# Performance work log

Measured on AMD Instinct MI355X. Metric: run time of the kernel, lower is better.

## Reference

```python
import jax, jax.numpy as jnp
import numpy as np

HIDDEN = 256
MAX_LENGTH = 256
NUM_LAYERS = 4
VOCAB = 50257


def setup_inputs() -> dict:
    key = jax.random.key(0)
    ks = jax.random.split(key, 16)
    s = 0.05
    return {
        "token": jax.random.randint(ks[0], (1,), 0, VOCAB, dtype=jnp.int64 if jax.config.jax_enable_x64 else jnp.int32),
        "hidden": jax.random.normal(ks[1], (NUM_LAYERS, 1, HIDDEN), dtype=jnp.float32),
        "encoder_outputs": jax.random.normal(ks[2], (MAX_LENGTH, HIDDEN), dtype=jnp.float32),
        "emb": jax.random.normal(ks[3], (VOCAB, HIDDEN), dtype=jnp.float32) * s,
        "attn_w": jax.random.normal(ks[4], (MAX_LENGTH, 2 * HIDDEN), dtype=jnp.float32) * s,
        "attn_b": jax.random.normal(ks[5], (MAX_LENGTH,), dtype=jnp.float32) * s,
        "comb_w": jax.random.normal(ks[6], (HIDDEN, 2 * HIDDEN), dtype=jnp.float32) * s,
        "comb_b": jax.random.normal(ks[7], (HIDDEN,), dtype=jnp.float32) * s,
        "gru_wih": jax.random.normal(ks[8], (NUM_LAYERS, 3 * HIDDEN, HIDDEN), dtype=jnp.float32) * s,
        "gru_whh": jax.random.normal(ks[9], (NUM_LAYERS, 3 * HIDDEN, HIDDEN), dtype=jnp.float32) * s,
        "gru_bih": jax.random.normal(ks[10], (NUM_LAYERS, 3 * HIDDEN), dtype=jnp.float32) * s,
        "gru_bhh": jax.random.normal(ks[11], (NUM_LAYERS, 3 * HIDDEN), dtype=jnp.float32) * s,
        "out_w": jax.random.normal(ks[12], (VOCAB, HIDDEN), dtype=jnp.float32) * s,
        "out_b": jax.random.normal(ks[13], (VOCAB,), dtype=jnp.float32) * s,
    }


def _gru_cell(x, h, wih, whh, bih, bhh):
    # PyTorch GRU cell: gates ordered [r, z, n]
    gi = x @ wih.T + bih  # [1, 3H]
    gh = h @ whh.T + bhh  # [1, 3H]
    i_r, i_z, i_n = jnp.split(gi, 3, axis=1)
    h_r, h_z, h_n = jnp.split(gh, 3, axis=1)
    r = jax.nn.sigmoid(i_r + h_r)
    z = jax.nn.sigmoid(i_z + h_z)
    n = jnp.tanh(i_n + r * h_n)
    return (1.0 - z) * n + z * h


def reference(token, hidden, encoder_outputs, emb, attn_w, attn_b, comb_w, comb_b,
              gru_wih, gru_whh, gru_bih, gru_bhh, out_w, out_b):
    # embedding lookup (dropout is identity in eval)  -> [1, H]
    embedded = emb[token]
    # Bahdanau-style attention weights over MAX_LENGTH positions
    attn_in = jnp.concatenate([embedded, hidden[0]], axis=1)  # [1, 2H]
    attn_weights = jax.nn.softmax(attn_in @ attn_w.T + attn_b, axis=1)  # [1, L]
    attn_applied = attn_weights @ encoder_outputs  # [1, H]
    comb_in = jnp.concatenate([embedded, attn_applied], axis=1)  # [1, 2H]
    x = jax.nn.relu(comb_in @ comb_w.T + comb_b)  # [1, H]
    # 4-layer GRU, single timestep
    new_h = []
    for l in range(NUM_LAYERS):
        h_l = _gru_cell(x, hidden[l], gru_wih[l], gru_whh[l], gru_bih[l], gru_bhh[l])
        new_h.append(h_l)
        x = h_l
    hidden_new = jnp.stack(new_h, axis=0)  # [4, 1, H]
    logp = jax.nn.log_softmax(x @ out_w.T + out_b, axis=1)  # [1, V]
    return (logp, hidden_new, attn_weights)
```

## Files before the change

kernel.cpp:

```cpp
#include <hip/hip_runtime.h>
#include <hip/hip_bf16.h>

#define H 256
#define L2H 512
#define NLAYERS 4
#define VOCAB 50257

#define OUT_LOGP 0
#define OUT_HID  50257
#define OUT_ATTN 51281

#define WS_SCORE 0
#define WS_BARS  256
#define WS_APP   512
#define WS_XA    768
#define WS_XB    1024
#define WS_PM    768
#define WS_PS    1024
#define WS_X4    1280
#define WS_GO    2048
#define WS_FLAG  2304

#define PH_SCORE 0
#define PH_APP   1
#define PH_X0    2
#define PH_LOG   7

#define NCHAIN 64
#define NBLK   256

typedef unsigned short u16;
typedef unsigned long long u64;

__device__ __forceinline__ float bf2f(u16 u) {
    return __uint_as_float(((unsigned int)u) << 16);
}

__device__ __forceinline__ u16 f2bf(float f) {
    unsigned int x = __float_as_uint(f);
    unsigned int r = x + 0x7fff + ((x >> 16) & 1);
    return (u16)(r >> 16);
}

template<bool BF16>
__device__ __forceinline__ float ld1(const void* p, size_t i) {
    if (BF16) return bf2f(((const u16*)p)[i]);
    else      return ((const float*)p)[i];
}

template<bool BF16>
__device__ __forceinline__ float4 ld4(const void* p, size_t i) {
    if (BF16) {
        ushort4 w = *(const ushort4*)((const u16*)p + i);
        return make_float4(bf2f(w.x), bf2f(w.y), bf2f(w.z), bf2f(w.w));
    } else {
        return *(const float4*)((const float*)p + i);
    }
}

template<bool BF16>
__device__ __forceinline__ void ld8(const void* p, size_t i, float* f) {
    if (BF16) {
        uint4 u = *(const uint4*)((const u16*)p + i);
        f[0] = bf2f(u.x & 0xffff); f[1] = bf2f(u.x >> 16);
        f[2] = bf2f(u.y & 0xffff); f[3] = bf2f(u.y >> 16);
        f[4] = bf2f(u.z & 0xffff); f[5] = bf2f(u.z >> 16);
        f[6] = bf2f(u.w & 0xffff); f[7] = bf2f(u.w >> 16);
    } else {
        const float4* q = (const float4*)((const float*)p + i);
        float4 a = q[0], b = q[1];
        f[0] = a.x; f[1] = a.y; f[2] = a.z; f[3] = a.w;
        f[4] = b.x; f[5] = b.y; f[6] = b.z; f[7] = b.w;
    }
}

template<bool BF16>
__device__ __forceinline__ void st(void* p, size_t i, float v) {
    if (BF16) ((u16*)p)[i] = f2bf(v);
    else      ((float*)p)[i] = v;
}

__device__ __forceinline__ float ldc(const float* p) {
    return __hip_atomic_load(const_cast<float*>(p), __ATOMIC_RELAXED, __HIP_MEMORY_SCOPE_AGENT);
}
__device__ __forceinline__ void stc(float* p, float v) {
    __hip_atomic_store(p, v, __ATOMIC_RELAXED, __HIP_MEMORY_SCOPE_AGENT);
}
__device__ __forceinline__ u64 ldcu(const u64* p) {
    return __hip_atomic_load(const_cast<u64*>(p), __ATOMIC_RELAXED, __HIP_MEMORY_SCOPE_AGENT);
}
__device__ __forceinline__ void stcu(u64* p, u64 v) {
    __hip_atomic_store(p, v, __ATOMIC_RELAXED, __HIP_MEMORY_SCOPE_AGENT);
}

__device__ __forceinline__ void stage256(float* sh, const float* src, int tid) {
    if (tid < 128) {
        u64 u = ldcu((const u64*)src + tid);
        sh[2 * tid]     = __uint_as_float((unsigned)(u & 0xffffffffull));
        sh[2 * tid + 1] = __uint_as_float((unsigned)(u >> 32));
    }
    __syncthreads();
}

__device__ __forceinline__ void arrive_ph(unsigned* bars, int bx, int ph) {
    __syncthreads();
    if (threadIdx.x == 0)
        __hip_atomic_fetch_add(&bars[(bx & 15) * 16 + ph], 1u,
                               __ATOMIC_RELAXED, __HIP_MEMORY_SCOPE_AGENT);
}
template<int SLP>
__device__ __forceinline__ void wait_ph(unsigned* bars, int ph, unsigned exp) {
    if (threadIdx.x < 16) {
        while (__hip_atomic_load(&bars[threadIdx.x * 16 + ph],
                                 __ATOMIC_RELAXED, __HIP_MEMORY_SCOPE_AGENT) < exp)
            __builtin_amdgcn_s_sleep(SLP);
    }
    __syncthreads();
}

template<int SLP>
__device__ __forceinline__ u64 poll_go(const u64* p, unsigned need) {
    u64 u = ldcu(p);
    while ((unsigned)(u & 0xffffffffull) < need) {
        __builtin_amdgcn_s_sleep(SLP);
        u = ldcu(p);
    }
    return u;
}

__device__ __forceinline__ float dot8_u4bf(uint4 u, const float* xf) {
    return bf2f(u.x & 0xffff)*xf[0] + bf2f(u.x >> 16)*xf[1]
         + bf2f(u.y & 0xffff)*xf[2] + bf2f(u.y >> 16)*xf[3]
         + bf2f(u.z & 0xffff)*xf[4] + bf2f(u.z >> 16)*xf[5]
         + bf2f(u.w & 0xffff)*xf[6] + bf2f(u.w >> 16)*xf[7];
}

__global__ __launch_bounds__(256) void k_init(const void* emb, float* ws) {
    int tid = threadIdx.x;
    __hip_atomic_store((unsigned*)(ws + WS_BARS) + tid, 0u, __ATOMIC_RELAXED, __HIP_MEMORY_SCOPE_AGENT);
    __hip_atomic_store((unsigned*)(ws + WS_GO) + tid, 0u, __ATOMIC_RELAXED, __HIP_MEMORY_SCOPE_AGENT);
    __hip_atomic_store((unsigned*)(ws + WS_APP) + tid, 0u, __ATOMIC_RELAXED, __HIP_MEMORY_SCOPE_AGENT);
    if (tid < 64) {
        float b = fabsf(bf2f(((const u16*)emb)[tid]));
        #pragma unroll
        for (int off = 32; off; off >>= 1) b = fmaxf(b, __shfl_xor(b, off));
        if (tid == 0) ws[WS_FLAG] = (b < 1.0f) ? 1.0f : 0.0f;
    }
}

template<bool BF16>
__device__ __forceinline__ void logits_stream(
    const void* __restrict__ out_w, const void* __restrict__ out_b,
    const float* xf, int grp, int l32, float* vs, float& m, float& s)
{
    #pragma unroll
    for (int it = 0; it < 3; ++it) {
        const int rb = it * 16384 + grp;
        float wf[8][8], bb[8];
        #pragma unroll
        for (int k = 0; k < 8; ++k) {
            ld8<BF16>(out_w, (size_t)(rb + (k << 11)) * H + l32 * 8, wf[k]);
            bb[k] = ld1<BF16>(out_b, rb + (k << 11));
        }
        #pragma unroll
        for (int k = 0; k < 8; ++k) {
            float v = wf[k][0]*xf[0] + wf[k][1]*xf[1] + wf[k][2]*xf[2] + wf[k][3]*xf[3]
                    + wf[k][4]*xf[4] + wf[k][5]*xf[5] + wf[k][6]*xf[6] + wf[k][7]*xf[7];
            #pragma unroll
            for (int off = 16; off; off >>= 1) v += __shfl_xor(v, off);
            v += bb[k];
            vs[it * 8 + k] = v;
            float mn = fmaxf(m, v);
            s = s * __expf(m - mn) + __expf(v - mn);
            m = mn;
        }
    }
    vs[24] = 0.f;
    if (grp < VOCAB - 49152) {
        int r = 49152 + grp;
        float wf[8]; ld8<BF16>(out_w, (size_t)r * H + l32 * 8, wf);
        float v = wf[0]*xf[0] + wf[1]*xf[1] + wf[2]*xf[2] + wf[3]*xf[3]
                + wf[4]*xf[4] + wf[5]*xf[5] + wf[6]*xf[6] + wf[7]*xf[7];
        #pragma unroll
        for (int off = 16; off; off >>= 1) v += __shfl_xor(v, off);
        v += ld1<BF16>(out_b, r);
        vs[24] = v;
        float mn = fmaxf(m, v);
        s = s * __expf(m - mn) + __expf(v - mn);
        m = mn;
    }
}

template<bool BF16>
__device__ __forceinline__ void pipeline(
    const int* __restrict__ tok, const void* __restrict__ emb,
    const void* __restrict__ hidden,
    const void* __restrict__ attn_w, const void* __restrict__ attn_b,
    const void* __restrict__ enc,
    const void* __restrict__ comb_w, const void* __restrict__ comb_b,
    const void* __restrict__ gwih, const void* __restrict__ gwhh,
    const void* __restrict__ gbih, const void* __restrict__ gbhh,
    const void* __restrict__ out_w, const void* __restrict__ out_b,
    float* __restrict__ ws, void* __restrict__ out)
{
    unsigned* bars = (unsigned*)(ws + WS_BARS);
    const int tid  = threadIdx.x;
    const int lane = tid & 63;
    const int wid  = tid >> 6;
    const int bx   = blockIdx.x;
    const size_t es = BF16 ? 2 : 4;

    const int grp = (bx << 3) | (tid >> 5);
    const int l32 = tid & 31;

    __shared__ float lds[256];
    __shared__ float xsh[256];
    __shared__ float wsm[256];
    __shared__ float cshare;

    float vs[25];
    float m = -1e30f, s = 0.f;

    if (bx < NCHAIN) {
        const int wv = (bx << 2) | wid;
        const int j8 = lane * 8;
        const int tk = tok[0];

        {
            float wf[8]; ld8<BF16>(attn_w, (size_t)wv * L2H + j8, wf);
            float xin[8];
            if (lane < 32) ld8<BF16>(emb, (size_t)tk * H + j8, xin);
            else           ld8<BF16>(hidden, (size_t)(j8 - H), xin);
            float v = 0.f;
            #pragma unroll
            for (int q = 0; q < 8; ++q) v += xin[q] * wf[q];
            #pragma unroll
            for (int off = 32; off; off >>= 1) v += __shfl_xor(v, off);
            if (lane == 0) stc(ws + WS_SCORE + wv, v + ld1<BF16>(attn_b, wv));
        }
        arrive_ph(bars, bx, PH_SCORE);

        if (bx < 16) {
            const int l0 = bx * 16;
            float ev[16];
            #pragma unroll
            for (int k = 0; k < 16; ++k)
                ev[k] = ld1<BF16>(enc, (size_t)(l0 + k) * H + tid);
            wait_ph<1>(bars, PH_SCORE, 4);
            stage256(lds, ws + WS_SCORE, tid);
            float sc = lds[tid];
            __syncthreads();
            for (int off = 128; off; off >>= 1) {
                if (tid < off) lds[tid] = fmaxf(lds[tid], lds[tid + off]);
                __syncthreads();
            }
            float M = lds[0]; __syncthreads();
            float e = __expf(sc - M);
            lds[tid] = e; __syncthreads();
            for (int off = 128; off; off >>= 1) {
                if (tid < off) lds[tid] += lds[tid + off];
                __syncthreads();
            }
            float w = e / lds[0];
            wsm[tid] = w; __syncthreads();
            if (bx == 0) st<BF16>(out, OUT_ATTN + tid, w);
            float acc = 0.f;
            #pragma unroll
            for (int k = 0; k < 16; ++k) acc += wsm[l0 + k] * ev[k];
            atomicAdd(&ws[WS_APP + tid], acc);
            arrive_ph(bars, bx, PH_APP);
        }

        {
            float wf[8]; ld8<BF16>(comb_w, (size_t)wv * L2H + j8, wf);
            float xin[8];
            if (lane < 32) ld8<BF16>(emb, (size_t)tk * H + j8, xin);
            wait_ph<1>(bars, PH_APP, 1);
            stage256(xsh, ws + WS_APP, tid);
            if (lane >= 32) {
                #pragma unroll
                for (int q = 0; q < 8; ++q) xin[q] = xsh[j8 - H + q];
            }
            float v = 0.f;
            #pragma unroll
            for (int q = 0; q < 8; ++q) v += xin[q] * wf[q];
            #pragma unroll
            for (int off = 32; off; off >>= 1) v += __shfl_xor(v, off);
            if (lane == 0) stc(ws + WS_XA + wv, fmaxf(v + ld1<BF16>(comb_b, wv), 0.f));
        }
        arrive_ph(bars, bx, PH_X0);

        const int e4 = lane * 4;
        #pragma unroll 1
        for (int l = 0; l < NLAYERS; ++l) {
            const float* xin_p = ws + ((l & 1) ? WS_XB : WS_XA);
            float*       xout  = ws + ((l & 1) ? WS_XA : WS_XB);
            const char* wih = (const char*)gwih + (size_t)l * 3 * H * H * es;
            const char* whh = (const char*)gwhh + (size_t)l * 3 * H * H * es;
            const char* bih = (const char*)gbih + (size_t)l * 3 * H * es;
            const char* bhh = (const char*)gbhh + (size_t)l * 3 * H * es;
            const char* hprev = (const char*)hidden + (size_t)l * H * es;
            char*       hout  = (char*)out + (size_t)(OUT_HID + l * H) * es;
            const int i = wv;

            float4 hv  = ld4<BF16>(hprev, e4);
            float4 wri = ld4<BF16>(wih, (size_t)(i        ) * H + e4);
            float4 wzi = ld4<BF16>(wih, (size_t)(H + i    ) * H + e4);
            float4 wni = ld4<BF16>(wih, (size_t)(2 * H + i) * H + e4);
            float4 wrh = ld4<BF16>(whh, (size_t)(i        ) * H + e4);
            float4 wzh = ld4<BF16>(whh, (size_t)(H + i    ) * H + e4);
            float4 wnh = ld4<BF16>(whh, (size_t)(2 * H + i) * H + e4);

            wait_ph<1>(bars, PH_X0 + l, 4);
            stage256(xsh, xin_p, tid);

            float4 xv;
            xv.x = xsh[e4]; xv.y = xsh[e4 + 1]; xv.z = xsh[e4 + 2]; xv.w = xsh[e4 + 3];

            float a = wri.x * xv.x + wri.y * xv.y + wri.z * xv.z + wri.w * xv.w
                    + wrh.x * hv.x + wrh.y * hv.y + wrh.z * hv.z + wrh.w * hv.w;
            float b = wzi.x * xv.x + wzi.y * xv.y + wzi.z * xv.z + wzi.w * xv.w
                    + wzh.x * hv.x + wzh.y * hv.y + wzh.z * hv.z + wzh.w * hv.w;
            float c = wni.x * xv.x + wni.y * xv.y + wni.z * xv.z + wni.w * xv.w;
            float d = wnh.x * hv.x + wnh.y * hv.y + wnh.z * hv.z + wnh.w * hv.w;

            #pragma unroll
            for (int off = 32; off; off >>= 1) {
                a += __shfl_xor(a, off);
                b += __shfl_xor(b, off);
                c += __shfl_xor(c, off);
                d += __shfl_xor(d, off);
            }
            if (lane == 0) {
                float r = 1.f / (1.f + __expf(-(a + ld1<BF16>(bih, i) + ld1<BF16>(bhh, i))));
                float z = 1.f / (1.f + __expf(-(b + ld1<BF16>(bih, H + i) + ld1<BF16>(bhh, H + i))));
                float n = tanhf(c + ld1<BF16>(bih, 2 * H + i) + r * (d + ld1<BF16>(bhh, 2 * H + i)));
                float hold = ld1<BF16>(hprev, i);
                float hn = (1.f - z) * n + z * hold;
                if (l < 3) stc(xout + i, hn);
                else {
                    stc(ws + WS_X4 + i, hn);
                    stc(ws + WS_X4 + 256 + i, hn);
                    stc(ws + WS_X4 + 512 + i, hn);
                }
                st<BF16>(hout, i, hn);
            }
            arrive_ph(bars, bx, PH_X0 + l + 1);
        }

        wait_ph<1>(bars, PH_X0 + 4, 4);
        if (bx < 16 && tid == 0)
            stcu((u64*)(ws + WS_GO + 16 * bx), 1ull);

        stage256(xsh, ws + WS_X4 + (bx % 3) * 256, tid);
        float xf[8];
        #pragma unroll
        for (int q = 0; q < 8; ++q) xf[q] = xsh[l32 * 8 + q];
        logits_stream<BF16>(out_w, out_b, xf, grp, l32, vs, m, s);
    } else {
        if constexpr (BF16) {
            uint4 pw[25]; float pb[25];
            #pragma unroll
            for (int it = 0; it < 3; ++it)
                #pragma unroll
                for (int k = 0; k < 8; ++k) {
                    int r = it * 16384 + (k << 11) + grp;
                    pw[it * 8 + k] = *(const uint4*)((const u16*)out_w + (size_t)r * H + l32 * 8);
                    pb[it * 8 + k] = ld1<true>(out_b, r);
                }
            if (grp < VOCAB - 49152) {
                int r = 49152 + grp;
                pw[24] = *(const uint4*)((const u16*)out_w + (size_t)r * H + l32 * 8);
                pb[24] = ld1<true>(out_b, r);
            } else { pw[24] = make_uint4(0, 0, 0, 0); pb[24] = 0.f; }

            if (tid == 0) (void)poll_go<2>((const u64*)(ws + WS_GO + 16 * (bx & 15)), 1u);
            __syncthreads();
            stage256(xsh, ws + WS_X4 + (bx % 3) * 256, tid);
            float xf[8];
            #pragma unroll
            for (int q = 0; q < 8; ++q) xf[q] = xsh[l32 * 8 + q];

            #pragma unroll
            for (int idx = 0; idx < 24; ++idx) {
                float v = dot8_u4bf(pw[idx], xf);
                #pragma unroll
                for (int off = 16; off; off >>= 1) v += __shfl_xor(v, off);
                v += pb[idx];
                vs[idx] = v;
                float mn = fmaxf(m, v);
                s = s * __expf(m - mn) + __expf(v - mn);
                m = mn;
            }
            vs[24] = 0.f;
            if (grp < VOCAB - 49152) {
                float v = dot8_u4bf(pw[24], xf);
                #pragma unroll
                for (int off = 16; off; off >>= 1) v += __shfl_xor(v, off);
                v += pb[24];
                vs[24] = v;
                float mn = fmaxf(m, v);
                s = s * __expf(m - mn) + __expf(v - mn);
                m = mn;
            }
        } else {
            if (tid == 0) (void)poll_go<2>((const u64*)(ws + WS_GO + 16 * (bx & 15)), 1u);
            __syncthreads();
            stage256(xsh, ws + WS_X4 + (bx % 3) * 256, tid);
            float xf[8];
            #pragma unroll
            for (int q = 0; q < 8; ++q) xf[q] = xsh[l32 * 8 + q];
            logits_stream<false>(out_w, out_b, xf, grp, l32, vs, m, s);
        }
    }

    {
        float mo = __shfl_xor(m, 32), so = __shfl_xor(s, 32);
        float M = fmaxf(m, mo);
        s = s * __expf(m - M) + so * __expf(mo - M);
        m = M;
    }
    __syncthreads();
    if (lane == 0) { lds[wid] = m; lds[4 + wid] = s; }
    __syncthreads();
    if (tid == 0) {
        float M01 = fmaxf(lds[0], lds[1]);
        float S01 = lds[4] * __expf(lds[0] - M01) + lds[5] * __expf(lds[1] - M01);
        float M23 = fmaxf(lds[2], lds[3]);
        float S23 = lds[6] * __expf(lds[2] - M23) + lds[7] * __expf(lds[3] - M23);
        float Mx = fmaxf(M01, M23);
        float S  = S01 * __expf(M01 - Mx) + S23 * __expf(M23 - Mx);
        stc(ws + WS_PM + bx, Mx);
        stc(ws + WS_PS + bx, S);
    }
    arrive_ph(bars, bx, PH_LOG);

    float c;
    if (bx == 0) {
        if (tid < 16) {
            while (__hip_atomic_load(&bars[tid * 16 + PH_LOG],
                                     __ATOMIC_RELAXED, __HIP_MEMORY_SCOPE_AGENT) < 16u)
                __builtin_amdgcn_s_sleep(1);
        }
        __syncthreads();
        float mm = ldc(ws + WS_PM + tid);
        float ss = ldc(ws + WS_PS + tid);
        #pragma unroll
        for (int off = 32; off; off >>= 1) {
            float mo = __shfl_xor(mm, off), so = __shfl_xor(ss, off);
            float M = fmaxf(mm, mo);
            ss = ss * __expf(mm - M) + so * __expf(mo - M);
            mm = M;
        }
        if (lane == 0) { lds[wid] = mm; lds[4 + wid] = ss; }
        __syncthreads();
        if (tid == 0) {
            float M01 = fmaxf(lds[0], lds[1]);
            float S01 = lds[4] * __expf(lds[0] - M01) + lds[5] * __expf(lds[1] - M01);
            float M23 = fmaxf(lds[2], lds[3]);
            float S23 = lds[6] * __expf(lds[2] - M23) + lds[7] * __expf(lds[3] - M23);
            float Mx = fmaxf(M01, M23);
            float S  = S01 * __expf(M01 - Mx) + S23 * __expf(M23 - Mx);
            cshare = Mx + __logf(S);
        }
        __syncthreads();
        c = cshare;
        if (tid < 16)
            stcu((u64*)(ws + WS_GO + 16 * tid),
                 ((u64)__float_as_uint(c) << 32) | 2ull);
    } else {
        if (tid == 0) {
            u64 u = poll_go<2>((const u64*)(ws + WS_GO + 16 * (bx & 15)), 2u);
            cshare = __uint_as_float((unsigned)(u >> 32));
        }
        __syncthreads();
        c = cshare;
    }

    if (l32 == 0) {
        #pragma unroll
        for (int it = 0; it < 3; ++it)
            #pragma unroll
            for (int k = 0; k < 8; ++k)
                st<BF16>(out, OUT_LOGP + it * 16384 + (k << 11) + grp, vs[it * 8 + k] - c);
        if (grp < VOCAB - 49152)
            st<BF16>(out, OUT_LOGP + 49152 + grp, vs[24] - c);
    }
}

__global__ __launch_bounds__(256, 1) void k_all(
    const int* __restrict__ tok, const void* __restrict__ emb,
    const void* __restrict__ hidden,
    const void* __restrict__ attn_w, const void* __restrict__ attn_b,
    const void* __restrict__ enc,
    const void* __restrict__ comb_w, const void* __restrict__ comb_b,
    const void* __restrict__ gwih, const void* __restrict__ gwhh,
    const void* __restrict__ gbih, const void* __restrict__ gbhh,
    const void* __restrict__ out_w, const void* __restrict__ out_b,
    float* __restrict__ ws, void* __restrict__ out)
{
    if (ws[WS_FLAG] > 0.5f)
        pipeline<true >(tok, emb, hidden, attn_w, attn_b, enc, comb_w, comb_b,
                        gwih, gwhh, gbih, gbhh, out_w, out_b, ws, out);
    else
        pipeline<false>(tok, emb, hidden, attn_w, attn_b, enc, comb_w, comb_b,
                        gwih, gwhh, gbih, gbhh, out_w, out_b, ws, out);
}

extern "C" void kernel_launch(void* const* d_in, const int* in_sizes, int n_in,
                              void* d_out, int out_size, void* d_ws, size_t ws_size,
                              hipStream_t stream) {
    const int* tok = (const int*)d_in[0];
    float* ws = (float*)d_ws;

    k_init<<<dim3(1), dim3(256), 0, stream>>>(d_in[3], ws);
    k_all<<<dim3(NBLK), dim3(256), 0, stream>>>(
        tok, d_in[3], d_in[1], d_in[4], d_in[5], d_in[2], d_in[6], d_in[7],
        d_in[8], d_in[9], d_in[10], d_in[11], d_in[12], d_in[13],
        ws, d_out);
}
```

Baseline: 160.4 us.

## Move bf16 logits onto non-chain blocks and replicate GRU state buffers

In the bf16 path the 64 chain blocks no longer compute logits. The remaining 192 blocks each prefetch 33 rows of out_w into registers before the GRU finishes, so the vocab projection is spread over idle blocks whose loads overlap the serial chain. The attention softmax now uses wave shuffles instead of LDS tree reductions, and the attn_applied atomics become a deterministic per-block reduction, which drops the zeroing in init. GRU hidden states are written to two buffers so that different blocks read different addresses, and the relay reducer moves to block 64. The cost is higher register pressure from 33 prefetched uint4 rows per thread and a more intricate workspace layout with aliased slots.

New measurement: 161.8 us. About the same (+0.8%).

```diff
diff --git a/kernel.cpp b/kernel.cpp
--- a/kernel.cpp
+++ b/kernel.cpp
@@ -15,11 +15,12 @@
 #define WS_APP   512
 #define WS_XA    768
 #define WS_XB    1024
-#define WS_PM    768
-#define WS_PS    1024
 #define WS_X4    1280
 #define WS_GO    2048
 #define WS_FLAG  2304
+
+#define WS_PM    1024
+#define WS_PS    0
 
 #define PH_SCORE 0
 #define PH_APP   1
@@ -28,6 +29,9 @@
 
 #define NCHAIN 64
 #define NBLK   256
+#define RELAY  64
+#define PROWS  33
+#define PSTRIDE 1536
 
 typedef unsigned short u16;
 typedef unsigned long long u64;
@@ -139,7 +143,6 @@
     int tid = threadIdx.x;
     __hip_atomic_store((unsigned*)(ws + WS_BARS) + tid, 0u, __ATOMIC_RELAXED, __HIP_MEMORY_SCOPE_AGENT);
     __hip_atomic_store((unsigned*)(ws + WS_GO) + tid, 0u, __ATOMIC_RELAXED, __HIP_MEMORY_SCOPE_AGENT);
-    __hip_atomic_store((unsigned*)(ws + WS_APP) + tid, 0u, __ATOMIC_RELAXED, __HIP_MEMORY_SCOPE_AGENT);
     if (tid < 64) {
         float b = fabsf(bf2f(((const u16*)emb)[tid]));
         #pragma unroll
@@ -209,16 +212,14 @@
     const int wid  = tid >> 6;
     const int bx   = blockIdx.x;
     const size_t es = BF16 ? 2 : 4;
-
-    const int grp = (bx << 3) | (tid >> 5);
-    const int l32 = tid & 31;
+    const int l32  = tid & 31;
 
     __shared__ float lds[256];
     __shared__ float xsh[256];
     __shared__ float wsm[256];
     __shared__ float cshare;
 
-    float vs[25];
+    float vs[PROWS];
     float m = -1e30f, s = 0.f;
 
     if (bx < NCHAIN) {
@@ -241,33 +242,45 @@
         arrive_ph(bars, bx, PH_SCORE);
 
         if (bx < 16) {
-            const int l0 = bx * 16;
+            const int cl = tid & 15;
+            const int g  = tid >> 4;
+            const int col = bx * 16 + cl;
             float ev[16];
             #pragma unroll
             for (int k = 0; k < 16; ++k)
-                ev[k] = ld1<BF16>(enc, (size_t)(l0 + k) * H + tid);
+                ev[k] = ld1<BF16>(enc, (size_t)(g * 16 + k) * H + col);
             wait_ph<1>(bars, PH_SCORE, 4);
             stage256(lds, ws + WS_SCORE, tid);
             float sc = lds[tid];
             __syncthreads();
-            for (int off = 128; off; off >>= 1) {
-                if (tid < off) lds[tid] = fmaxf(lds[tid], lds[tid + off]);
-                __syncthreads();
-            }
-            float M = lds[0]; __syncthreads();
+            float wm = sc;
+            #pragma unroll
+            for (int off = 32; off; off >>= 1) wm = fmaxf(wm, __shfl_xor(wm, off));
+            if (lane == 0) lds[wid] = wm;
+            __syncthreads();
+            float M = fmaxf(fmaxf(lds[0], lds[1]), fmaxf(lds[2], lds[3]));
             float e = __expf(sc - M);
-            lds[tid] = e; __syncthreads();
-            for (int off = 128; off; off >>= 1) {
-                if (tid < off) lds[tid] += lds[tid + off];
-                __syncthreads();
-            }
-            float w = e / lds[0];
-            wsm[tid] = w; __syncthreads();
+            float esum = e;
+            #pragma unroll
+            for (int off = 32; off; off >>= 1) esum += __shfl_xor(esum, off);
+            if (lane == 0) lds[4 + wid] = esum;
+            __syncthreads();
+            float S = (lds[4] + lds[5]) + (lds[6] + lds[7]);
+            float w = e / S;
+            wsm[tid] = w;
+            __syncthreads();
             if (bx == 0) st<BF16>(out, OUT_ATTN + tid, w);
             float acc = 0.f;
             #pragma unroll
-            for (int k = 0; k < 16; ++k) acc += wsm[l0 + k] * ev[k];
-            atomicAdd(&ws[WS_APP + tid], acc);
+            for (int k = 0; k < 16; ++k) acc += wsm[g * 16 + k] * ev[k];
+            lds[tid] = acc;
+            __syncthreads();
+            if (tid < 16) {
+                float a = 0.f;
+                #pragma unroll
+                for (int gg = 0; gg < 16; ++gg) a += lds[gg * 16 + tid];
+                stc(ws + WS_APP + bx * 16 + tid, a);
+            }
             arrive_ph(bars, bx, PH_APP);
         }
 
@@ -286,15 +299,19 @@
             for (int q = 0; q < 8; ++q) v += xin[q] * wf[q];
             #pragma unroll
             for (int off = 32; off; off >>= 1) v += __shfl_xor(v, off);
-            if (lane == 0) stc(ws + WS_XA + wv, fmaxf(v + ld1<BF16>(comb_b, wv), 0.f));
+            if (lane == 0) {
+                float x0 = fmaxf(v + ld1<BF16>(comb_b, wv), 0.f);
+                stc(ws + WS_XA + wv, x0);
+                stc(ws + WS_SCORE + wv, x0);
+            }
         }
         arrive_ph(bars, bx, PH_X0);
 
         const int e4 = lane * 4;
         #pragma unroll 1
         for (int l = 0; l < NLAYERS; ++l) {
-            const float* xin_p = ws + ((l & 1) ? WS_XB : WS_XA);
-            float*       xout  = ws + ((l & 1) ? WS_XA : WS_XB);
+            const float* xsrc = (l & 1) ? ((bx & 1) ? ws + WS_XB : ws + WS_APP)
+                                        : ((bx & 1) ? ws + WS_XA : ws + WS_SCORE);
             const char* wih = (const char*)gwih + (size_t)l * 3 * H * H * es;
             const char* whh = (const char*)gwhh + (size_t)l * 3 * H * H * es;
             const char* bih = (const char*)gbih + (size_t)l * 3 * H * es;
@@ -312,7 +329,7 @@
             float4 wnh = ld4<BF16>(whh, (size_t)(2 * H + i) * H + e4);
 
             wait_ph<1>(bars, PH_X0 + l, 4);
-            stage256(xsh, xin_p, tid);
+            stage256(xsh, xsrc, tid);
 
             float4 xv;
             xv.x = xsh[e4]; xv.y = xsh[e4 + 1]; xv.z = xsh[e4 + 2]; xv.w = xsh[e4 + 3];
@@ -337,8 +354,12 @@
                 float n = tanhf(c + ld1<BF16>(bih, 2 * H + i) + r * (d + ld1<BF16>(bhh, 2 * H + i)));
                 float hold = ld1<BF16>(hprev, i);
                 float hn = (1.f - z) * n + z * hold;
-                if (l < 3) stc(xout + i, hn);
-                else {
+                if (l < 3) {
+                    float* prim = (l & 1) ? ws + WS_XA : ws + WS_XB;
+                    float* repl = (l & 1) ? ws + WS_SCORE : ws + WS_APP;
+                    stc(prim + i, hn);
+                    stc(repl + i, hn);
+                } else {
                     stc(ws + WS_X4 + i, hn);
                     stc(ws + WS_X4 + 256 + i, hn);
                     stc(ws + WS_X4 + 512 + i, hn);
@@ -352,27 +373,36 @@
         if (bx < 16 && tid == 0)
             stcu((u64*)(ws + WS_GO + 16 * bx), 1ull);
 
-        stage256(xsh, ws + WS_X4 + (bx % 3) * 256, tid);
-        float xf[8];
-        #pragma unroll
-        for (int q = 0; q < 8; ++q) xf[q] = xsh[l32 * 8 + q];
-        logits_stream<BF16>(out_w, out_b, xf, grp, l32, vs, m, s);
+        if constexpr (BF16) {
+            if (tid == 0) {
+                stc(ws + WS_PM + bx, -1e30f);
+                stc(ws + WS_PS + bx, 0.f);
+            }
+            arrive_ph(bars, bx, PH_LOG);
+            return;
+        } else {
+            stage256(xsh, ws + WS_X4 + (bx % 3) * 256, tid);
+            float xf[8];
+            #pragma unroll
+            for (int q = 0; q < 8; ++q) xf[q] = xsh[l32 * 8 + q];
+            const int grp = (bx << 3) | (tid >> 5);
+            logits_stream<false>(out_w, out_b, xf, grp, l32, vs, m, s);
+        }
     } else {
         if constexpr (BF16) {
-            uint4 pw[25]; float pb[25];
-            #pragma unroll
-            for (int it = 0; it < 3; ++it)
-                #pragma unroll
-                for (int k = 0; k < 8; ++k) {
-                    int r = it * 16384 + (k << 11) + grp;
-                    pw[it * 8 + k] = *(const uint4*)((const u16*)out_w + (size_t)r * H + l32 * 8);
-                    pb[it * 8 + k] = ld1<true>(out_b, r);
-                }
-            if (grp < VOCAB - 49152) {
-                int r = 49152 + grp;
-                pw[24] = *(const uint4*)((const u16*)out_w + (size_t)r * H + l32 * 8);
-                pb[24] = ld1<true>(out_b, r);
-            } else { pw[24] = make_uint4(0, 0, 0, 0); pb[24] = 0.f; }
+            const int pgrp = ((bx - 64) << 3) | (tid >> 5);
+            uint4 pw[PROWS]; float pb[PROWS];
+            #pragma unroll
+            for (int k = 0; k < 32; ++k) {
+                int r = k * PSTRIDE + pgrp;
+                pw[k] = *(const uint4*)((const u16*)out_w + (size_t)r * H + l32 * 8);
+                pb[k] = ld1<true>(out_b, r);
+            }
+            if (pgrp < VOCAB - 32 * PSTRIDE) {
+                int r = 32 * PSTRIDE + pgrp;
+                pw[32] = *(const uint4*)((const u16*)out_w + (size_t)r * H + l32 * 8);
+                pb[32] = ld1<true>(out_b, r);
+            } else { pw[32] = make_uint4(0, 0, 0, 0); pb[32] = 0.f; }
 
             if (tid == 0) (void)poll_go<2>((const u64*)(ws + WS_GO + 16 * (bx & 15)), 1u);
             __syncthreads();
@@ -382,23 +412,23 @@
             for (int q = 0; q < 8; ++q) xf[q] = xsh[l32 * 8 + q];
 
             #pragma unroll
-            for (int idx = 0; idx < 24; ++idx) {
-                float v = dot8_u4bf(pw[idx], xf);
+            for (int k = 0; k < 32; ++k) {
+                float v = dot8_u4bf(pw[k], xf);
                 #pragma unroll
                 for (int off = 16; off; off >>= 1) v += __shfl_xor(v, off);
-                v += pb[idx];
-                vs[idx] = v;
+                v += pb[k];
+                vs[k] = v;
                 float mn = fmaxf(m, v);
                 s = s * __expf(m - mn) + __expf(v - mn);
                 m = mn;
             }
-            vs[24] = 0.f;
-            if (grp < VOCAB - 49152) {
-                float v = dot8_u4bf(pw[24], xf);
+            vs[32] = 0.f;
+            if (pgrp < VOCAB - 32 * PSTRIDE) {
+                float v = dot8_u4bf(pw[32], xf);
                 #pragma unroll
                 for (int off = 16; off; off >>= 1) v += __shfl_xor(v, off);
-                v += pb[24];
-                vs[24] = v;
+                v += pb[32];
+                vs[32] = v;
                 float mn = fmaxf(m, v);
                 s = s * __expf(m - mn) + __expf(v - mn);
                 m = mn;
@@ -410,6 +440,7 @@
             float xf[8];
             #pragma unroll
             for (int q = 0; q < 8; ++q) xf[q] = xsh[l32 * 8 + q];
+            const int grp = (bx << 3) | (tid >> 5);
             logits_stream<false>(out_w, out_b, xf, grp, l32, vs, m, s);
         }
     }
@@ -436,7 +467,7 @@
     arrive_ph(bars, bx, PH_LOG);
 
     float c;
-    if (bx == 0) {
+    if (bx == RELAY) {
         if (tid < 16) {
             while (__hip_atomic_load(&bars[tid * 16 + PH_LOG],
                                      __ATOMIC_RELAXED, __HIP_MEMORY_SCOPE_AGENT) < 16u)
@@ -477,14 +508,26 @@
         c = cshare;
     }
 
-    if (l32 == 0) {
-        #pragma unroll
-        for (int it = 0; it < 3; ++it)
-            #pragma unroll
-            for (int k = 0; k < 8; ++k)
-                st<BF16>(out, OUT_LOGP + it * 16384 + (k << 11) + grp, vs[it * 8 + k] - c);
-        if (grp < VOCAB - 49152)
-            st<BF16>(out, OUT_LOGP + 49152 + grp, vs[24] - c);
+    if constexpr (BF16) {
+        const int pgrp = ((bx - 64) << 3) | (tid >> 5);
+        if (l32 == 0) {
+            #pragma unroll
+            for (int k = 0; k < 32; ++k)
+                st<true>(out, OUT_LOGP + k * PSTRIDE + pgrp, vs[k] - c);
+            if (pgrp < VOCAB - 32 * PSTRIDE)
+                st<true>(out, OUT_LOGP + 32 * PSTRIDE + pgrp, vs[32] - c);
+        }
+    } else {
+        const int grp = (bx << 3) | (tid >> 5);
+        if (l32 == 0) {
+            #pragma unroll
+            for (int it = 0; it < 3; ++it)
+                #pragma unroll
+                for (int k = 0; k < 8; ++k)
+                    st<false>(out, OUT_LOGP + it * 16384 + (k << 11) + grp, vs[it * 8 + k] - c);
+            if (grp < VOCAB - 49152)
+                st<false>(out, OUT_LOGP + 49152 + grp, vs[24] - c);
+        }
     }
 }
 
```
